# Optimization experiments

Measured on AMD Instinct MI355X. Metric: run time of the kernel, lower is better.

Reference implementation:

```python
import jax, jax.numpy as jnp
import numpy as np
from jax import lax

B, T, IN, H = 4096, 512, 11, 16


def lstm(x, Wih, Whh, bih, bhh):
    # x: [B, T, in]; PyTorch gate order i, f, g, o packed along 4H.
    xg = jnp.einsum('bti,gi->btg', x, Wih) + bih + bhh  # [B, T, 4H]
    h0 = jnp.zeros((x.shape[0], Whh.shape[1]), x.dtype)
    c0 = jnp.zeros_like(h0)

    def step(carry, xg_t):
        h, c = carry
        g = xg_t + h @ Whh.T                      # [B, 4H]
        i, f, gg, o = jnp.split(g, 4, axis=-1)
        i = jax.nn.sigmoid(i)
        f = jax.nn.sigmoid(f)
        gg = jnp.tanh(gg)
        o = jax.nn.sigmoid(o)
        c = f * c + i * gg
        h = o * jnp.tanh(c)
        return (h, c), h

    _, hs = lax.scan(step, (h0, c0), jnp.swapaxes(xg, 0, 1))  # hs: [T, B, H]
    return jnp.swapaxes(hs, 0, 1)  # [B, T, H]


def setup_inputs() -> dict:
    key = jax.random.key(0)
    ks = jax.random.split(key, 16)
    s = 1.0 / np.sqrt(H)
    u = lambda k, shape: jax.random.uniform(k, shape, jnp.float32, -s, s)
    return {
        'x': jax.random.normal(ks[0], (B, T, IN), jnp.float32),
        'Wih1': u(ks[1], (4 * H, IN)), 'Whh1': u(ks[2], (4 * H, H)),
        'bih1': u(ks[3], (4 * H,)), 'bhh1': u(ks[4], (4 * H,)),
        'Wih2': u(ks[5], (4 * H, H)), 'Whh2': u(ks[6], (4 * H, H)),
        'bih2': u(ks[7], (4 * H,)), 'bhh2': u(ks[8], (4 * H,)),
        'Wd1': u(ks[9], (8, H)), 'bd1': u(ks[10], (8,)),
        'Wd2': u(ks[11], (8, 8)), 'bd2': u(ks[12], (8,)),
        'Wd3': u(ks[13], (3, 8)), 'bd3': u(ks[14], (3,)),
    }


def reference(x, Wih1, Whh1, bih1, bhh1, Wih2, Whh2, bih2, bhh2,
              Wd1, bd1, Wd2, bd2, Wd3, bd3):
    h1 = lstm(x, Wih1, Whh1, bih1, bhh1)          # [B, T, H]
    # Dropout2d treated as identity (eval mode).
    h2 = lstm(h1, Wih2, Whh2, bih2, bhh2)          # [B, T, H]
    s = jax.nn.softmax(h2, axis=1)[:, -1, :]       # softmax over TIME, take last step -> [B, H]
    d = (s @ Wd1.T + bd1) @ Wd2.T + bd2
    d = d @ Wd3.T + bd3                            # [B, 3]
    return jax.nn.softmax(d, axis=1)
```

## Files before the change

kernel.cpp:

```cpp
#include <hip/hip_runtime.h>

#define T_STEPS 512
#define IN_DIM 11
#define ROW_PAD 12
#define H_DIM 16
#define ROW_F (T_STEPS * IN_DIM)
#define CHUNK_T 16
#define CHUNK_F (CHUNK_T * IN_DIM)
#define N_CHUNK (T_STEPS / CHUNK_T)
#define LOG2E 1.44269504088896340736f

typedef float v2f __attribute__((ext_vector_type(2)));

__device__ __forceinline__ v2f pk_fma(v2f a, v2f b, v2f c) {
    v2f d;
    asm("v_pk_fma_f32 %0, %1, %2, %3" : "=v"(d) : "v"(a), "v"(b), "v"(c));
    return d;
}

template<int CTRL>
__device__ __forceinline__ float qperm(float v) {
    return __builtin_bit_cast(float,
        __builtin_amdgcn_update_dpp(0, __builtin_bit_cast(int, v),
                                    CTRL, 0xf, 0xf, true));
}

__device__ __forceinline__ float bcast_lane(float v, int l) {
    return __builtin_bit_cast(float,
        __builtin_amdgcn_readlane(__builtin_bit_cast(int, v), l));
}

__global__ __launch_bounds__(256, 4) void lstm2_head(
    const float* __restrict__ x,
    const float* __restrict__ Wih1, const float* __restrict__ Whh1,
    const float* __restrict__ bih1, const float* __restrict__ bhh1,
    const float* __restrict__ Wih2, const float* __restrict__ Whh2,
    const float* __restrict__ bih2, const float* __restrict__ bhh2,
    const float* __restrict__ Wd1, const float* __restrict__ bd1,
    const float* __restrict__ Wd2, const float* __restrict__ bd2,
    const float* __restrict__ Wd3, const float* __restrict__ bd3,
    float* __restrict__ out)
{
    __shared__ float xlds[4][2][212];
    __shared__ v2f   shh[4][2][8];

    const int lane = threadIdx.x & 63;
    const int wid = __builtin_amdgcn_readfirstlane((int)(threadIdx.x >> 6));
    const int b = blockIdx.x * 4 + wid;

    const int r   = lane >> 2;
    const int gt  = lane & 3;
    const int row = gt * H_DIM + r;

    const bool is_t = (gt == 2);
    const float M   = is_t ? (-2.0f * LOG2E) : (-LOG2E);
    const float vAa = is_t ? 2.0f : 1.0f;
    const float vBc = is_t ? -1.0f : 0.0f;

    v2f wi1p[6], wh1p[8], wi2p[8], wh2p[8];
    #pragma unroll
    for (int j = 0; j < 5; ++j)
        wi1p[j] = (v2f){M * Wih1[row * IN_DIM + 2 * j], M * Wih1[row * IN_DIM + 2 * j + 1]};
    wi1p[5] = (v2f){M * Wih1[row * IN_DIM + 10], 0.0f};
    #pragma unroll
    for (int j = 0; j < 8; ++j) {
        wh1p[j] = (v2f){M * Whh1[row * H_DIM + 2 * j], M * Whh1[row * H_DIM + 2 * j + 1]};
        wi2p[j] = (v2f){M * Wih2[row * H_DIM + 2 * j], M * Wih2[row * H_DIM + 2 * j + 1]};
        wh2p[j] = (v2f){M * Whh2[row * H_DIM + 2 * j], M * Whh2[row * H_DIM + 2 * j + 1]};
    }
    const float bb1 = M * (bih1[row] + bhh1[row]);
    const float bb2 = M * (bih2[row] + bhh2[row]);
    #pragma unroll
    for (int j = 0; j < 6; ++j) asm volatile("" : "+v"(wi1p[j]));
    #pragma unroll
    for (int j = 0; j < 8; ++j) {
        asm volatile("" : "+v"(wh1p[j]));
        asm volatile("" : "+v"(wi2p[j]));
        asm volatile("" : "+v"(wh2p[j]));
    }

    const float* __restrict__ xb = x + (size_t)b * ROW_F;
    float* const xl0 = &xlds[wid][0][0];
    float* const xl1 = &xlds[wid][1][0];
    v2f* const h1mem = &shh[wid][0][0];
    v2f* const h2mem = &shh[wid][1][0];

    if (lane < 16) { h1mem[lane >> 1] = (v2f){0.f, 0.f}; }
    ((float*)h1mem)[r & 15] = 0.0f;
    ((float*)h2mem)[r & 15] = 0.0f;
    if (lane < 32) {
        const int buf = lane >> 4, rr = lane & 15;
        xlds[wid][buf][rr * ROW_PAD + IN_DIM] = 0.0f;
    }

    const int f1i = lane, f2i = lane + 64, f3i = lane + 128;
    const int p1 = (f1i / IN_DIM) * ROW_PAD + (f1i % IN_DIM);
    const int p2 = (f2i / IN_DIM) * ROW_PAD + (f2i % IN_DIM);
    const int p3 = (f3i / IN_DIM) * ROW_PAD + (f3i % IN_DIM);

    float gl0 = xb[f1i];
    float gl1 = xb[f2i];
    float gl2 = xb[min(f3i, ROW_F - 1)];

    float c1 = 0.f, c2 = 0.f, h2v = 0.f, ssum = 0.f;
    v2f h1r[8], h2r[8];
    #pragma unroll
    for (int j = 0; j < 8; ++j) { h1r[j] = (v2f){0.f, 0.f}; h2r[j] = (v2f){0.f, 0.f}; }

    for (int ck = 0; ck < N_CHUNK; ++ck) {
        float* const xbuf = (ck & 1) ? xl1 : xl0;
        xbuf[p1] = gl0;
        xbuf[p2] = gl1;
        xbuf[p3] = gl2;
        if (ck + 1 < N_CHUNK) {
            const int base = (ck + 1) * CHUNK_F;
            gl0 = xb[base + f1i];
            gl1 = xb[base + f2i];
            gl2 = xb[min(base + f3i, ROW_F - 1)];
        }

        #pragma unroll
        for (int t2 = 0; t2 < CHUNK_T; ++t2) {
            const v2f* const xr = (const v2f*)(xbuf + t2 * ROW_PAD);

            v2f a2p = pk_fma(wh2p[0], h2r[0], (v2f){bb2, 0.f});
            #pragma unroll
            for (int j = 1; j < 8; ++j) a2p = pk_fma(wh2p[j], h2r[j], a2p);

            v2f a1p = pk_fma(wi1p[0], xr[0], (v2f){bb1, 0.f});
            #pragma unroll
            for (int j = 1; j < 6; ++j) a1p = pk_fma(wi1p[j], xr[j], a1p);
            #pragma unroll
            for (int j = 0; j < 8; ++j) a1p = pk_fma(wh1p[j], h1r[j], a1p);

            const float g1 = a1p.x + a1p.y;
            const float a1 = __builtin_fmaf(vAa,
                __builtin_amdgcn_rcpf(1.0f + __builtin_amdgcn_exp2f(g1)), vBc);
            {
                const float gi = qperm<0x00>(a1);
                const float gf = qperm<0x55>(a1);
                const float gg = qperm<0xAA>(a1);
                const float go = qperm<0xFF>(a1);
                c1 = __builtin_fmaf(gf, c1, gi * gg);
                const float tc = __builtin_fmaf(2.0f,
                    __builtin_amdgcn_rcpf(1.0f +
                        __builtin_amdgcn_exp2f(-2.0f * LOG2E * c1)), -1.0f);
                ((float*)h1mem)[r] = go * tc;
            }
            #pragma unroll
            for (int j = 0; j < 8; ++j) h1r[j] = h1mem[j];

            #pragma unroll
            for (int j = 0; j < 8; ++j) a2p = pk_fma(wi2p[j], h1r[j], a2p);

            const float g2 = a2p.x + a2p.y;
            const float a2 = __builtin_fmaf(vAa,
                __builtin_amdgcn_rcpf(1.0f + __builtin_amdgcn_exp2f(g2)), vBc);
            {
                const float gi = qperm<0x00>(a2);
                const float gf = qperm<0x55>(a2);
                const float gg = qperm<0xAA>(a2);
                const float go = qperm<0xFF>(a2);
                c2 = __builtin_fmaf(gf, c2, gi * gg);
                const float tc = __builtin_fmaf(2.0f,
                    __builtin_amdgcn_rcpf(1.0f +
                        __builtin_amdgcn_exp2f(-2.0f * LOG2E * c2)), -1.0f);
                h2v = go * tc;
                ((float*)h2mem)[r] = h2v;
            }
            #pragma unroll
            for (int j = 0; j < 8; ++j) h2r[j] = h2mem[j];

            ssum += __builtin_amdgcn_exp2f(LOG2E * h2v);
        }
    }

    const float sv = __builtin_amdgcn_exp2f(LOG2E * h2v) / ssum;

    float ssb[H_DIM];
    #pragma unroll
    for (int k = 0; k < H_DIM; ++k) ssb[k] = bcast_lane(sv, 4 * k);

    const int r8 = lane & 7;
    float acc1 = bd1[r8];
    #pragma unroll
    for (int k = 0; k < H_DIM; ++k)
        acc1 = __builtin_fmaf(Wd1[r8 * H_DIM + k], ssb[k], acc1);

    float d1s[8];
    #pragma unroll
    for (int j = 0; j < 8; ++j) d1s[j] = bcast_lane(acc1, j);

    float acc2 = bd2[r8];
    #pragma unroll
    for (int k = 0; k < 8; ++k)
        acc2 = __builtin_fmaf(Wd2[r8 * 8 + k], d1s[k], acc2);

    float d2s[8];
    #pragma unroll
    for (int j = 0; j < 8; ++j) d2s[j] = bcast_lane(acc2, j);

    float lg = 0.f;
    if (lane < 3) {
        lg = bd3[lane];
        #pragma unroll
        for (int k = 0; k < 8; ++k)
            lg = __builtin_fmaf(Wd3[lane * 8 + k], d2s[k], lg);
    }
    const float l0 = bcast_lane(lg, 0);
    const float l1 = bcast_lane(lg, 1);
    const float l2 = bcast_lane(lg, 2);
    const float mx = fmaxf(l0, fmaxf(l1, l2));
    const float e0 = __builtin_amdgcn_exp2f(LOG2E * (l0 - mx));
    const float e1 = __builtin_amdgcn_exp2f(LOG2E * (l1 - mx));
    const float e2 = __builtin_amdgcn_exp2f(LOG2E * (l2 - mx));
    const float inv = 1.0f / (e0 + e1 + e2);
    if (lane < 3) {
        const float ev = (lane == 0) ? e0 : ((lane == 1) ? e1 : e2);
        out[b * 3 + lane] = ev * inv;
    }
}

extern "C" void kernel_launch(void* const* d_in, const int* in_sizes, int n_in,
                              void* d_out, int out_size, void* d_ws, size_t ws_size,
                              hipStream_t stream) {
    (void)in_sizes; (void)n_in; (void)out_size; (void)d_ws; (void)ws_size;
    const float* x    = (const float*)d_in[0];
    const float* Wih1 = (const float*)d_in[1];
    const float* Whh1 = (const float*)d_in[2];
    const float* bih1 = (const float*)d_in[3];
    const float* bhh1 = (const float*)d_in[4];
    const float* Wih2 = (const float*)d_in[5];
    const float* Whh2 = (const float*)d_in[6];
    const float* bih2 = (const float*)d_in[7];
    const float* bhh2 = (const float*)d_in[8];
    const float* Wd1  = (const float*)d_in[9];
    const float* bd1  = (const float*)d_in[10];
    const float* Wd2  = (const float*)d_in[11];
    const float* bd2  = (const float*)d_in[12];
    const float* Wd3  = (const float*)d_in[13];
    const float* bd3  = (const float*)d_in[14];

    lstm2_head<<<dim3(4096 / 4), dim3(256), 0, stream>>>(
        x, Wih1, Whh1, bih1, bhh1, Wih2, Whh2, bih2, bhh2,
        Wd1, bd1, Wd2, bd2, Wd3, bd3, (float*)d_out);
}
```

Baseline: 455.2 us.

## Switch LSTM gate matvecs to fp16 dot2 with half-precision LDS state

```diff
diff --git a/kernel.cpp b/kernel.cpp
--- a/kernel.cpp
+++ b/kernel.cpp
@@ -10,13 +10,20 @@
 #define N_CHUNK (T_STEPS / CHUNK_T)
 #define LOG2E 1.44269504088896340736f
 
-typedef float v2f __attribute__((ext_vector_type(2)));
-
-__device__ __forceinline__ v2f pk_fma(v2f a, v2f b, v2f c) {
-    v2f d;
-    asm("v_pk_fma_f32 %0, %1, %2, %3" : "=v"(d) : "v"(a), "v"(b), "v"(c));
+typedef _Float16 v2h __attribute__((ext_vector_type(2)));
+typedef _Float16 v8h __attribute__((ext_vector_type(8)));
+
+#if __has_builtin(__builtin_amdgcn_fdot2)
+__device__ __forceinline__ float fdot2(v2h a, v2h b, float c) {
+    return __builtin_amdgcn_fdot2(a, b, c, false);
+}
+#else
+__device__ __forceinline__ float fdot2(v2h a, v2h b, float c) {
+    float d;
+    asm("v_dot2_f32_f16 %0, %1, %2, %3" : "=v"(d) : "v"(a), "v"(b), "v"(c));
     return d;
 }
+#endif
 
 template<int CTRL>
 __device__ __forceinline__ float qperm(float v) {
@@ -30,7 +37,9 @@
         __builtin_amdgcn_readlane(__builtin_bit_cast(int, v), l));
 }
 
-__global__ __launch_bounds__(256, 4) void lstm2_head(
+__global__ __launch_bounds__(256)
+__attribute__((amdgpu_waves_per_eu(4, 4)))
+void lstm2_head(
     const float* __restrict__ x,
     const float* __restrict__ Wih1, const float* __restrict__ Whh1,
     const float* __restrict__ bih1, const float* __restrict__ bhh1,
@@ -41,8 +50,8 @@
     const float* __restrict__ Wd3, const float* __restrict__ bd3,
     float* __restrict__ out)
 {
-    __shared__ float xlds[4][2][212];
-    __shared__ v2f   shh[4][2][8];
+    __shared__ _Float16 xlds[4][2][216];
+    __shared__ v8h      shh8[4][2][2];
 
     const int lane = threadIdx.x & 63;
     const int wid = __builtin_amdgcn_readfirstlane((int)(threadIdx.x >> 6));
@@ -57,40 +66,43 @@
     const float vAa = is_t ? 2.0f : 1.0f;
     const float vBc = is_t ? -1.0f : 0.0f;
 
-    v2f wi1p[6], wh1p[8], wi2p[8], wh2p[8];
+    v2h wi1h[6], wh1h[8], wi2h[8], wh2h[8];
     #pragma unroll
     for (int j = 0; j < 5; ++j)
-        wi1p[j] = (v2f){M * Wih1[row * IN_DIM + 2 * j], M * Wih1[row * IN_DIM + 2 * j + 1]};
-    wi1p[5] = (v2f){M * Wih1[row * IN_DIM + 10], 0.0f};
+        wi1h[j] = (v2h){(_Float16)(M * Wih1[row * IN_DIM + 2 * j]),
+                        (_Float16)(M * Wih1[row * IN_DIM + 2 * j + 1])};
+    wi1h[5] = (v2h){(_Float16)(M * Wih1[row * IN_DIM + 10]), (_Float16)0.0f};
     #pragma unroll
     for (int j = 0; j < 8; ++j) {
-        wh1p[j] = (v2f){M * Whh1[row * H_DIM + 2 * j], M * Whh1[row * H_DIM + 2 * j + 1]};
-        wi2p[j] = (v2f){M * Wih2[row * H_DIM + 2 * j], M * Wih2[row * H_DIM + 2 * j + 1]};
-        wh2p[j] = (v2f){M * Whh2[row * H_DIM + 2 * j], M * Whh2[row * H_DIM + 2 * j + 1]};
+        wh1h[j] = (v2h){(_Float16)(M * Whh1[row * H_DIM + 2 * j]),
+                        (_Float16)(M * Whh1[row * H_DIM + 2 * j + 1])};
+        wi2h[j] = (v2h){(_Float16)(M * Wih2[row * H_DIM + 2 * j]),
+                        (_Float16)(M * Wih2[row * H_DIM + 2 * j + 1])};
+        wh2h[j] = (v2h){(_Float16)(M * Whh2[row * H_DIM + 2 * j]),
+                        (_Float16)(M * Whh2[row * H_DIM + 2 * j + 1])};
     }
     const float bb1 = M * (bih1[row] + bhh1[row]);
     const float bb2 = M * (bih2[row] + bhh2[row]);
     #pragma unroll
-    for (int j = 0; j < 6; ++j) asm volatile("" : "+v"(wi1p[j]));
+    for (int j = 0; j < 6; ++j) asm volatile("" : "+v"(wi1h[j]));
     #pragma unroll
     for (int j = 0; j < 8; ++j) {
-        asm volatile("" : "+v"(wh1p[j]));
-        asm volatile("" : "+v"(wi2p[j]));
-        asm volatile("" : "+v"(wh2p[j]));
+        asm volatile("" : "+v"(wh1h[j]));
+        asm volatile("" : "+v"(wi2h[j]));
+        asm volatile("" : "+v"(wh2h[j]));
     }
 
     const float* __restrict__ xb = x + (size_t)b * ROW_F;
-    float* const xl0 = &xlds[wid][0][0];
-    float* const xl1 = &xlds[wid][1][0];
-    v2f* const h1mem = &shh[wid][0][0];
-    v2f* const h2mem = &shh[wid][1][0];
-
-    if (lane < 16) { h1mem[lane >> 1] = (v2f){0.f, 0.f}; }
-    ((float*)h1mem)[r & 15] = 0.0f;
-    ((float*)h2mem)[r & 15] = 0.0f;
+    _Float16* const xl0 = &xlds[wid][0][0];
+    _Float16* const xl1 = &xlds[wid][1][0];
+    _Float16* const h1w = (_Float16*)&shh8[wid][0][0];
+    _Float16* const h2w = (_Float16*)&shh8[wid][1][0];
+
+    h1w[r] = (_Float16)0.0f;
+    h2w[r] = (_Float16)0.0f;
     if (lane < 32) {
         const int buf = lane >> 4, rr = lane & 15;
-        xlds[wid][buf][rr * ROW_PAD + IN_DIM] = 0.0f;
+        xlds[wid][buf][rr * ROW_PAD + IN_DIM] = (_Float16)0.0f;
     }
 
     const int f1i = lane, f2i = lane + 64, f3i = lane + 128;
@@ -103,15 +115,18 @@
     float gl2 = xb[min(f3i, ROW_F - 1)];
 
     float c1 = 0.f, c2 = 0.f, h2v = 0.f, ssum = 0.f;
-    v2f h1r[8], h2r[8];
-    #pragma unroll
-    for (int j = 0; j < 8; ++j) { h1r[j] = (v2f){0.f, 0.f}; h2r[j] = (v2f){0.f, 0.f}; }
+    v2h h1r[8], h2r[8];
+    #pragma unroll
+    for (int j = 0; j < 8; ++j) {
+        h1r[j] = (v2h){(_Float16)0.f, (_Float16)0.f};
+        h2r[j] = (v2h){(_Float16)0.f, (_Float16)0.f};
+    }
 
     for (int ck = 0; ck < N_CHUNK; ++ck) {
-        float* const xbuf = (ck & 1) ? xl1 : xl0;
-        xbuf[p1] = gl0;
-        xbuf[p2] = gl1;
-        xbuf[p3] = gl2;
+        _Float16* const xbuf = (ck & 1) ? xl1 : xl0;
+        xbuf[p1] = (_Float16)gl0;
+        xbuf[p2] = (_Float16)gl1;
+        xbuf[p3] = (_Float16)gl2;
         if (ck + 1 < N_CHUNK) {
             const int base = (ck + 1) * CHUNK_F;
             gl0 = xb[base + f1i];
@@ -121,55 +136,72 @@
 
         #pragma unroll
         for (int t2 = 0; t2 < CHUNK_T; ++t2) {
-            const v2f* const xr = (const v2f*)(xbuf + t2 * ROW_PAD);
-
-            v2f a2p = pk_fma(wh2p[0], h2r[0], (v2f){bb2, 0.f});
-            #pragma unroll
-            for (int j = 1; j < 8; ++j) a2p = pk_fma(wh2p[j], h2r[j], a2p);
-
-            v2f a1p = pk_fma(wi1p[0], xr[0], (v2f){bb1, 0.f});
-            #pragma unroll
-            for (int j = 1; j < 6; ++j) a1p = pk_fma(wi1p[j], xr[j], a1p);
-            #pragma unroll
-            for (int j = 0; j < 8; ++j) a1p = pk_fma(wh1p[j], h1r[j], a1p);
-
-            const float g1 = a1p.x + a1p.y;
-            const float a1 = __builtin_fmaf(vAa,
+            const v2h* const xr = (const v2h*)(xbuf + t2 * ROW_PAD);
+
+            float a2 = bb2, b2 = 0.f;
+            #pragma unroll
+            for (int j = 0; j < 4; ++j) {
+                a2 = fdot2(wh2h[j],     h2r[j],     a2);
+                b2 = fdot2(wh2h[j + 4], h2r[j + 4], b2);
+            }
+
+            float a1 = bb1, b1 = 0.f;
+            #pragma unroll
+            for (int j = 0; j < 3; ++j) {
+                a1 = fdot2(wi1h[j],     xr[j],     a1);
+                b1 = fdot2(wi1h[j + 3], xr[j + 3], b1);
+            }
+            #pragma unroll
+            for (int j = 0; j < 4; ++j) {
+                a1 = fdot2(wh1h[j],     h1r[j],     a1);
+                b1 = fdot2(wh1h[j + 4], h1r[j + 4], b1);
+            }
+
+            const float g1 = a1 + b1;
+            const float act1 = __builtin_fmaf(vAa,
                 __builtin_amdgcn_rcpf(1.0f + __builtin_amdgcn_exp2f(g1)), vBc);
             {
-                const float gi = qperm<0x00>(a1);
-                const float gf = qperm<0x55>(a1);
-                const float gg = qperm<0xAA>(a1);
-                const float go = qperm<0xFF>(a1);
+                const float gi = qperm<0x00>(act1);
+                const float gf = qperm<0x55>(act1);
+                const float gg = qperm<0xAA>(act1);
+                const float go = qperm<0xFF>(act1);
                 c1 = __builtin_fmaf(gf, c1, gi * gg);
                 const float tc = __builtin_fmaf(2.0f,
                     __builtin_amdgcn_rcpf(1.0f +
                         __builtin_amdgcn_exp2f(-2.0f * LOG2E * c1)), -1.0f);
-                ((float*)h1mem)[r] = go * tc;
-            }
-            #pragma unroll
-            for (int j = 0; j < 8; ++j) h1r[j] = h1mem[j];
-
-            #pragma unroll
-            for (int j = 0; j < 8; ++j) a2p = pk_fma(wi2p[j], h1r[j], a2p);
-
-            const float g2 = a2p.x + a2p.y;
-            const float a2 = __builtin_fmaf(vAa,
+                h1w[r] = (_Float16)(go * tc);
+            }
+            {
+                const v2h* hp = (const v2h*)h1w;
+                #pragma unroll
+                for (int j = 0; j < 8; ++j) h1r[j] = hp[j];
+            }
+            #pragma unroll
+            for (int j = 0; j < 4; ++j) {
+                a2 = fdot2(wi2h[j],     h1r[j],     a2);
+                b2 = fdot2(wi2h[j + 4], h1r[j + 4], b2);
+            }
+
+            const float g2 = a2 + b2;
+            const float act2 = __builtin_fmaf(vAa,
                 __builtin_amdgcn_rcpf(1.0f + __builtin_amdgcn_exp2f(g2)), vBc);
             {
-                const float gi = qperm<0x00>(a2);
-                const float gf = qperm<0x55>(a2);
-                const float gg = qperm<0xAA>(a2);
-                const float go = qperm<0xFF>(a2);
+                const float gi = qperm<0x00>(act2);
+                const float gf = qperm<0x55>(act2);
+                const float gg = qperm<0xAA>(act2);
+                const float go = qperm<0xFF>(act2);
                 c2 = __builtin_fmaf(gf, c2, gi * gg);
                 const float tc = __builtin_fmaf(2.0f,
                     __builtin_amdgcn_rcpf(1.0f +
                         __builtin_amdgcn_exp2f(-2.0f * LOG2E * c2)), -1.0f);
                 h2v = go * tc;
-                ((float*)h2mem)[r] = h2v;
-            }
-            #pragma unroll
-            for (int j = 0; j < 8; ++j) h2r[j] = h2mem[j];
+                h2w[r] = (_Float16)h2v;
+            }
+            {
+                const v2h* hp = (const v2h*)h2w;
+                #pragma unroll
+                for (int j = 0; j < 8; ++j) h2r[j] = hp[j];
+            }
 
             ssum += __builtin_amdgcn_exp2f(LOG2E * h2v);
         }
```

Result: no change. 455.3 us (+0.0%).
